# Kernel optimization log

Measured on AMD Instinct MI355X. Metric: run time of the kernel, lower is better.

The kernel has to match this reference:

```python
import jax, jax.numpy as jnp
import numpy as np

B, S, D = 2, 2048, 1024
H, HD = 16, 64  # num_heads, head_dim
EPS = 1e-6      # flax LayerNorm default
ROPE_BASE = 10000.0


def _layernorm(x, scale, bias=None, eps=EPS):
    mu = jnp.mean(x, axis=-1, keepdims=True)
    var = jnp.mean(jnp.square(x - mu), axis=-1, keepdims=True)
    y = (x - mu) * jax.lax.rsqrt(var + eps) * scale
    return y + bias if bias is not None else y


def _rotate_half(x):
    x1, x2 = x[..., : x.shape[-1] // 2], x[..., x.shape[-1] // 2 :]
    return jnp.concatenate((-x2, x1), axis=-1)


def _rope_tables(seq_len, head_dim, dtype):
    inv_freq = 1.0 / ROPE_BASE ** (jnp.arange(0, head_dim, 2, dtype=jnp.float32) / head_dim)
    t = jnp.arange(seq_len, dtype=jnp.float32)
    freqs = jnp.einsum('i,j->ij', t, inv_freq)          # [S, HD/2]
    emb = jnp.concatenate((freqs, freqs), axis=-1)      # [S, HD]
    return jnp.cos(emb).astype(dtype), jnp.sin(emb).astype(dtype)


def setup_inputs() -> dict:
    key = jax.random.key(0)
    ks = jax.random.split(key, 4)
    return {
        'x': jax.random.normal(ks[0], (B, S, D), dtype=jnp.float32),
        'w_qkv': jax.random.normal(ks[1], (D, 3 * D), dtype=jnp.float32) * (1.0 / np.sqrt(D)),
        'b_qkv': jnp.zeros((3 * D,), dtype=jnp.float32),
        'w_out': jax.random.normal(ks[2], (D, D), dtype=jnp.float32) * (0.1 / np.sqrt(D)),
        'b_out': jnp.zeros((D,), dtype=jnp.float32),
        'ln_scale': jnp.ones((D,), dtype=jnp.float32),
        'ln_bias': jnp.zeros((D,), dtype=jnp.float32),
        'q_scale': jnp.ones((HD,), dtype=jnp.float32),
        'k_scale': jnp.ones((HD,), dtype=jnp.float32),
    }


def reference(x, w_qkv, b_qkv, w_out, b_out, ln_scale, ln_bias, q_scale, k_scale):
    b, s, d = x.shape
    # input LayerNorm
    xn = _layernorm(x, ln_scale, ln_bias)
    # fused QKV projection
    qkv = xn @ w_qkv + b_qkv                              # [B, S, 3D]
    q, k, v = jnp.split(qkv, 3, axis=-1)
    def to_bhsd(t):
        return t.reshape(b, s, H, HD).transpose(0, 2, 1, 3)
    q, k, v = to_bhsd(q), to_bhsd(k), to_bhsd(v)          # [B, H, S, HD]
    # per-head QK LayerNorm (no bias)
    q = _layernorm(q, q_scale)
    k = _layernorm(k, k_scale)
    # RoPE
    cos, sin = _rope_tables(s, HD, q.dtype)               # [S, HD]
    cos, sin = cos[None, None], sin[None, None]
    q = q * cos + _rotate_half(q) * sin
    k = k * cos + _rotate_half(k) * sin
    # scaled dot-product attention (softmax over key positions)
    scale = 1.0 / np.sqrt(HD)
    scores = jnp.einsum('bhqd,bhkd->bhqk', q, k) * scale  # [B, H, S, S]
    probs = jax.nn.softmax(scores, axis=-1)
    attn = jnp.einsum('bhqk,bhkd->bhqd', probs, v)        # [B, H, S, HD]
    attn = attn.transpose(0, 2, 1, 3).reshape(b, s, d)
    return attn @ w_out + b_out
```

## Files before the change

### kernel.cpp

```cpp
#include <hip/hip_runtime.h>
#include <math.h>

#define BB 2
#define SS 2048
#define DD 1024
#define HH 16
#define HDD 64
static constexpr float EPS = 1e-6f;

typedef __bf16 bf16x8 __attribute__((ext_vector_type(8)));
typedef __bf16 bf16x4 __attribute__((ext_vector_type(4)));
typedef float f32x4 __attribute__((ext_vector_type(4)));
typedef __attribute__((address_space(1))) const unsigned int gas_u32;
typedef __attribute__((address_space(3))) unsigned int las_u32;

__device__ __forceinline__ unsigned short f2bf(float f) {
    unsigned int u = __float_as_uint(f);
    u = (u + 0x7FFFu + ((u >> 16) & 1u)) >> 16;
    return (unsigned short)u;
}

__device__ __forceinline__ uint2 pack4bf(float a, float b, float c, float d) {
    bf16x4 v;
    v[0] = (__bf16)a; v[1] = (__bf16)b; v[2] = (__bf16)c; v[3] = (__bf16)d;
    return *(uint2*)&v;
}

__device__ __forceinline__ void async_ld16(const unsigned short* g, unsigned short* l) {
    __builtin_amdgcn_global_load_lds((gas_u32*)g, (las_u32*)l, 16, 0, 0);
}

__global__ __launch_bounds__(256) void cast_transpose(const float* __restrict__ w,
                                                      unsigned short* __restrict__ wt,
                                                      int K, int N) {
    __shared__ float tile[32][36];
    const int n0 = blockIdx.x * 32;
    const int k0 = blockIdx.y * 32;
    const int t = threadIdx.x;
    const int r = t >> 3;
    const int c = (t & 7) * 4;
    *(float4*)&tile[r][c] = *(const float4*)(w + (size_t)(k0 + r) * N + n0 + c);
    __syncthreads();
    unsigned short o[4];
#pragma unroll
    for (int i = 0; i < 4; i++) o[i] = f2bf(tile[c + i][r]);
    *(uint2*)(wt + (size_t)(n0 + r) * K + k0 + c) = *(uint2*)o;
}

__global__ __launch_bounds__(256) void rope_tables(float* __restrict__ ctab,
                                                   float* __restrict__ stab) {
    const int idx = blockIdx.x * 256 + threadIdx.x;
    const int s = idx >> 5;
    const int i = idx & 31;
    const float ang = (float)s * exp2f(-(float)i * (13.287712379549449f / 32.f));
    ctab[idx] = cosf(ang);
    stab[idx] = sinf(ang);
}

__global__ __launch_bounds__(256) void ln_kernel(const float* __restrict__ x,
                                                 const float* __restrict__ scale,
                                                 const float* __restrict__ bias,
                                                 unsigned short* __restrict__ xn) {
    __shared__ float red[4];
    const int row = blockIdx.x;
    const int t = threadIdx.x;
    const float* xr = x + (size_t)row * DD + t * 4;

    float4 v = *(const float4*)xr;
    float s = v.x + v.y + v.z + v.w;
#pragma unroll
    for (int o = 32; o; o >>= 1) s += __shfl_xor(s, o);
    if ((t & 63) == 0) red[t >> 6] = s;
    __syncthreads();
    const float mu = (red[0] + red[1] + red[2] + red[3]) * (1.f / DD);

    float4 d = {v.x - mu, v.y - mu, v.z - mu, v.w - mu};
    float sq = d.x * d.x + d.y * d.y + d.z * d.z + d.w * d.w;
#pragma unroll
    for (int o = 32; o; o >>= 1) sq += __shfl_xor(sq, o);
    __syncthreads();
    if ((t & 63) == 0) red[t >> 6] = sq;
    __syncthreads();
    const float var = (red[0] + red[1] + red[2] + red[3]) * (1.f / DD);
    const float rstd = rsqrtf(var + EPS);

    const float4 sc = *(const float4*)(scale + t * 4);
    const float4 bi = *(const float4*)(bias + t * 4);
    unsigned short o[4];
    o[0] = f2bf(d.x * rstd * sc.x + bi.x);
    o[1] = f2bf(d.y * rstd * sc.y + bi.y);
    o[2] = f2bf(d.z * rstd * sc.z + bi.z);
    o[3] = f2bf(d.w * rstd * sc.w + bi.w);
    *(uint2*)(xn + (size_t)row * DD + t * 4) = *(uint2*)o;
}

__global__ __launch_bounds__(256) void gemm_mfma_bt(const unsigned short* __restrict__ A,
                                                    const unsigned short* __restrict__ Bt,
                                                    const float* __restrict__ bias,
                                                    float* __restrict__ C,
                                                    int M, int N, int K) {
    __shared__ __align__(16) unsigned short As[128][32];
    __shared__ __align__(16) unsigned short Bs[128][32];

    const int bm = blockIdx.y * 128;
    const int bn = blockIdx.x * 128;
    const int t = threadIdx.x;
    const int wv = t >> 6;
    const int ln = t & 63;
    const int m16 = ln & 15;
    const int quad = ln >> 4;
    const int wm = (wv >> 1) * 64;
    const int wn = (wv & 1) * 64;

    f32x4 acc[4][4];
#pragma unroll
    for (int i = 0; i < 4; i++)
#pragma unroll
        for (int j = 0; j < 4; j++) acc[i][j] = (f32x4){0.f, 0.f, 0.f, 0.f};

    const int srow = wv * 32 + (ln >> 2);
    const int sk = (ln & 3) * 8;
    const unsigned short* aptr = A + (size_t)(bm + srow) * K + sk;
    const unsigned short* bptr = Bt + (size_t)(bn + srow) * K + sk;
    unsigned short* al0 = &As[wv * 32][0];
    unsigned short* al1 = &As[wv * 32 + 16][0];
    unsigned short* bl0 = &Bs[wv * 32][0];
    unsigned short* bl1 = &Bs[wv * 32 + 16][0];

    for (int k0 = 0; k0 < K; k0 += 32) {
        __syncthreads();
        async_ld16(aptr, al0);
        async_ld16(aptr + 16 * (size_t)K, al1);
        async_ld16(bptr, bl0);
        async_ld16(bptr + 16 * (size_t)K, bl1);
        __syncthreads();

        bf16x8 af[4], bf[4];
#pragma unroll
        for (int i = 0; i < 4; i++)
            af[i] = *(const bf16x8*)&As[wm + i * 16 + m16][quad * 8];
#pragma unroll
        for (int j = 0; j < 4; j++)
            bf[j] = *(const bf16x8*)&Bs[wn + j * 16 + m16][quad * 8];
#pragma unroll
        for (int i = 0; i < 4; i++)
#pragma unroll
            for (int j = 0; j < 4; j++)
                acc[i][j] = __builtin_amdgcn_mfma_f32_16x16x32_bf16(af[i], bf[j], acc[i][j], 0, 0, 0);

        aptr += 32;
        bptr += 32;
    }

#pragma unroll
    for (int j = 0; j < 4; j++) {
        const int n = bn + wn + j * 16 + m16;
        const float bv = bias[n];
#pragma unroll
        for (int i = 0; i < 4; i++) {
            float* cp = C + (size_t)(bm + wm + i * 16 + quad * 4) * N + n;
#pragma unroll
            for (int r = 0; r < 4; r++)
                cp[(size_t)r * N] = acc[i][j][r] + bv;
        }
    }
}

__device__ __forceinline__ float wave_sum64(float x) {
#pragma unroll
    for (int o = 32; o; o >>= 1) x += __shfl_xor(x, o);
    return x;
}

__global__ __launch_bounds__(256) void head_ln_rope(const float* __restrict__ qkv,
                                                    const float* __restrict__ q_scale,
                                                    const float* __restrict__ k_scale,
                                                    const float* __restrict__ ctab,
                                                    const float* __restrict__ stab,
                                                    unsigned short* __restrict__ qt,
                                                    unsigned short* __restrict__ kt,
                                                    unsigned short* __restrict__ vt) {
    const int wave = (blockIdx.x * 256 + threadIdx.x) >> 6;
    const int lane = threadIdx.x & 63;
    const int h = wave & (HH - 1);
    const int row = wave >> 4;
    const int b = row >> 11;
    const int s = row & (SS - 1);

    const float* base = qkv + (size_t)row * (3 * DD) + h * HDD;
    const float qv = base[lane];
    const float kv = base[DD + lane];
    const float vv = base[2 * DD + lane];

    const float mq = wave_sum64(qv) * (1.f / 64.f);
    const float dq = qv - mq;
    const float varq = wave_sum64(dq * dq) * (1.f / 64.f);
    const float yq = dq * rsqrtf(varq + EPS) * q_scale[lane];

    const float mk = wave_sum64(kv) * (1.f / 64.f);
    const float dk = kv - mk;
    const float vark = wave_sum64(dk * dk) * (1.f / 64.f);
    const float yk = dk * rsqrtf(vark + EPS) * k_scale[lane];

    const int i = lane & 31;
    const float cv = ctab[s * 32 + i];
    const float sv = stab[s * 32 + i];
    const float pq = __shfl_xor(yq, 32);
    const float pk = __shfl_xor(yk, 32);
    const float rq = (lane < 32) ? -pq : pq;
    const float rk = (lane < 32) ? -pk : pk;
    const float oq = yq * cv + rq * sv;
    const float ok = yk * cv + rk * sv;

    const size_t oidx = (((size_t)(b * HH + h) * SS) + s) * HDD + lane;
    qt[oidx] = f2bf(oq * 0.18033688011112042f);
    kt[oidx] = f2bf(ok);
    vt[oidx] = f2bf(vv);
}

__global__ __launch_bounds__(256) void transpose_v(const unsigned short* __restrict__ vt,
                                                   unsigned short* __restrict__ vtT) {
    __shared__ unsigned short tile[64][72];
    const int bh = blockIdx.x >> 5;
    const int s0 = (blockIdx.x & 31) * 64;
    const int t = threadIdx.x;
    const int row = t >> 2;
    const int c0 = (t & 3) * 16;
    const unsigned short* src = vt + ((size_t)bh * SS + s0 + row) * HDD + c0;
    *(uint4*)&tile[row][c0]     = *(const uint4*)(src);
    *(uint4*)&tile[row][c0 + 8] = *(const uint4*)(src + 8);
    __syncthreads();
    unsigned short outv[16];
#pragma unroll
    for (int i = 0; i < 16; i++) outv[i] = tile[c0 + i][row];
    unsigned short* dst = vtT + ((size_t)bh * HDD + row) * SS + s0 + c0;
    *(uint4*)dst       = *(uint4*)&outv[0];
    *(uint4*)(dst + 8) = *(uint4*)&outv[8];
}

__global__ __launch_bounds__(256, 4) void attn_mfma(const unsigned short* __restrict__ qt,
                                                    const unsigned short* __restrict__ kt,
                                                    const unsigned short* __restrict__ vtT,
                                                    float* __restrict__ Opart,
                                                    float* __restrict__ lpart) {
    __shared__ __align__(16) unsigned short KsS[64 * 64];
    __shared__ __align__(16) unsigned short VsS[64 * 64];
    __shared__ __align__(16) unsigned short PbS[4][32 * 64];

    const int bh = blockIdx.x >> 4;
    const int q0 = (blockIdx.x & 15) * 128;
    const int ks = blockIdx.y;
    const int t = threadIdx.x;
    const int wq = t >> 6;
    const int lane = t & 63;
    const int m16 = lane & 15;
    const int quad = lane >> 4;
    const int m7 = m16 & 7;

    const int cs = quad ^ m7;
    const int koff = m16 * 64 + cs * 8;
    const int srow = t >> 2;
    const int sch = (t & 3) * 2;
    const int sw0 = srow * 64 + ((sch)     ^ (srow & 7)) * 8;
    const int sw1 = srow * 64 + ((sch + 1) ^ (srow & 7)) * 8;
    const int pwb = m16 * 64 + 4 * (quad & 1);
    const int qh = quad >> 1;

    bf16x8 qb[2][2];
#pragma unroll
    for (int u = 0; u < 2; u++) {
        const unsigned short* qp =
            qt + ((size_t)bh * SS + q0 + wq * 32 + u * 16 + m16) * HDD + quad * 8;
        qb[u][0] = *(const bf16x8*)qp;
        qb[u][1] = *(const bf16x8*)(qp + 32);
    }

    bf16x8 ones;
#pragma unroll
    for (int j = 0; j < 8; j++) ones[j] = (__bf16)1.0f;

    f32x4 O[2][4];
#pragma unroll
    for (int u = 0; u < 2; u++)
#pragma unroll
        for (int f = 0; f < 4; f++) O[u][f] = (f32x4){0.f, 0.f, 0.f, 0.f};
    f32x4 lacc[2] = {(f32x4){0.f, 0.f, 0.f, 0.f}, (f32x4){0.f, 0.f, 0.f, 0.f}};

    const unsigned short* kbase = kt + (size_t)bh * SS * HDD;
    const unsigned short* vbase = vtT + (size_t)bh * HDD * SS;
    const f32x4 cinit = (f32x4){-12.f, -12.f, -12.f, -12.f};

    const int kstart = ks * (SS / 2);
    for (int k0 = kstart; k0 < kstart + SS / 2; k0 += 64) {
        __syncthreads();
        {
            const unsigned short* ksrc = kbase + (size_t)(k0 + srow) * HDD + sch * 8;
            *(uint4*)&KsS[sw0] = *(const uint4*)ksrc;
            *(uint4*)&KsS[sw1] = *(const uint4*)(ksrc + 8);
            const unsigned short* vsrc = vbase + (size_t)srow * SS + k0 + sch * 8;
            *(uint4*)&VsS[sw0] = *(const uint4*)vsrc;
            *(uint4*)&VsS[sw1] = *(const uint4*)(vsrc + 8);
        }
        __syncthreads();

        f32x4 S[2][4];
#pragma unroll
        for (int g = 0; g < 4; g++) {
            const bf16x8 ka0 = *(const bf16x8*)&KsS[g * 1024 + koff];
            const bf16x8 ka1 = *(const bf16x8*)&KsS[g * 1024 + (koff ^ 32)];
#pragma unroll
            for (int u = 0; u < 2; u++) {
                f32x4 a = __builtin_amdgcn_mfma_f32_16x16x32_bf16(ka0, qb[u][0], cinit, 0, 0, 0);
                a = __builtin_amdgcn_mfma_f32_16x16x32_bf16(ka1, qb[u][1], a, 0, 0, 0);
                S[u][g] = a;
            }
        }

#pragma unroll
        for (int u = 0; u < 2; u++) {
#pragma unroll
            for (int g = 0; g < 4; g++) {
                const float p0 = exp2f(S[u][g][0]);
                const float p1 = exp2f(S[u][g][1]);
                const float p2 = exp2f(S[u][g][2]);
                const float p3 = exp2f(S[u][g][3]);
                *(uint2*)&PbS[wq][u * 1024 + pwb + ((2 * g + qh) ^ m7) * 8] =
                    pack4bf(p0, p1, p2, p3);
            }
        }
        asm volatile("s_waitcnt lgkmcnt(0)" ::: "memory");

        bf16x8 pb[2][2];
#pragma unroll
        for (int u = 0; u < 2; u++) {
            pb[u][0] = *(const bf16x8*)&PbS[wq][u * 1024 + koff];
            pb[u][1] = *(const bf16x8*)&PbS[wq][u * 1024 + (koff ^ 32)];
        }

#pragma unroll
        for (int u = 0; u < 2; u++) {
            lacc[u] = __builtin_amdgcn_mfma_f32_16x16x32_bf16(ones, pb[u][0], lacc[u], 0, 0, 0);
            lacc[u] = __builtin_amdgcn_mfma_f32_16x16x32_bf16(ones, pb[u][1], lacc[u], 0, 0, 0);
        }
#pragma unroll
        for (int f = 0; f < 4; f++) {
            const bf16x8 va0 = *(const bf16x8*)&VsS[f * 1024 + koff];
            const bf16x8 va1 = *(const bf16x8*)&VsS[f * 1024 + (koff ^ 32)];
#pragma unroll
            for (int u = 0; u < 2; u++) {
                O[u][f] = __builtin_amdgcn_mfma_f32_16x16x32_bf16(va0, pb[u][0], O[u][f], 0, 0, 0);
                O[u][f] = __builtin_amdgcn_mfma_f32_16x16x32_bf16(va1, pb[u][1], O[u][f], 0, 0, 0);
            }
        }
    }

    const int b_ = bh >> 4;
    const int h_ = bh & 15;
    float* obase0 = Opart + (size_t)ks * ((size_t)BB * SS * DD);
#pragma unroll
    for (int u = 0; u < 2; u++) {
        const int s_ = q0 + wq * 32 + u * 16 + m16;
        float* orow = obase0 + ((size_t)b_ * SS + s_) * DD + h_ * HDD;
#pragma unroll
        for (int f = 0; f < 4; f++)
            *(f32x4*)(orow + f * 16 + quad * 4) = O[u][f];
        if (quad == 0)
            lpart[ks * (32 * SS) + bh * SS + s_] = lacc[u][0];
    }
}

__global__ __launch_bounds__(256) void combine_attn(const float* __restrict__ Opart,
                                                    const float* __restrict__ lpart,
                                                    unsigned short* __restrict__ attn) {
    const int row = blockIdx.x;
    const int t = threadIdx.x;
    const int c = t * 4;
    const int h = t >> 4;
    const int b = row >> 11;
    const int s = row & (SS - 1);

    const size_t off = (size_t)row * DD + c;
    const float4 o0 = *(const float4*)(Opart + off);
    const float4 o1 = *(const float4*)(Opart + (size_t)BB * SS * DD + off);
    const int li = (b * HH + h) * SS + s;
    const float inv = 1.f / (lpart[li] + lpart[32 * SS + li]);

    *(uint2*)(attn + off) = pack4bf((o0.x + o1.x) * inv, (o0.y + o1.y) * inv,
                                    (o0.z + o1.z) * inv, (o0.w + o1.w) * inv);
}

extern "C" void kernel_launch(void* const* d_in, const int* in_sizes, int n_in,
                              void* d_out, int out_size, void* d_ws, size_t ws_size,
                              hipStream_t stream) {
    const float* x        = (const float*)d_in[0];
    const float* w_qkv    = (const float*)d_in[1];
    const float* b_qkv    = (const float*)d_in[2];
    const float* w_out    = (const float*)d_in[3];
    const float* b_out    = (const float*)d_in[4];
    const float* ln_scale = (const float*)d_in[5];
    const float* ln_bias  = (const float*)d_in[6];
    const float* q_scale  = (const float*)d_in[7];
    const float* k_scale  = (const float*)d_in[8];
    float* out = (float*)d_out;

    char* ws = (char*)d_ws;
    const size_t MB = 1024 * 1024;
    unsigned short* xn    = (unsigned short*)(ws + 0);
    float*          lpart = (float*)(ws + 8 * MB);
    float*          ctab  = (float*)(ws + 9 * MB);
    float*          stab  = (float*)(ws + 10 * MB);
    float*          qkv   = (float*)(ws + 16 * MB);
    float*          Opart = (float*)(ws + 16 * MB);
    unsigned short* wqkvT = (unsigned short*)(ws + 64 * MB);
    unsigned short* woutT = (unsigned short*)(ws + 70 * MB);
    unsigned short* qt    = (unsigned short*)(ws + 72 * MB);
    unsigned short* kt    = (unsigned short*)(ws + 80 * MB);
    unsigned short* vt    = (unsigned short*)(ws + 88 * MB);
    unsigned short* vtT   = (unsigned short*)(ws + 96 * MB);
    unsigned short* attn  = (unsigned short*)(ws + 104 * MB);

    const int M = BB * SS;

    cast_transpose<<<dim3(3 * DD / 32, DD / 32), 256, 0, stream>>>(w_qkv, wqkvT, DD, 3 * DD);
    cast_transpose<<<dim3(DD / 32, DD / 32), 256, 0, stream>>>(w_out, woutT, DD, DD);
    rope_tables<<<SS * 32 / 256, 256, 0, stream>>>(ctab, stab);

    ln_kernel<<<M, 256, 0, stream>>>(x, ln_scale, ln_bias, xn);

    gemm_mfma_bt<<<dim3(3 * DD / 128, M / 128), 256, 0, stream>>>(xn, wqkvT, b_qkv, qkv,
                                                                  M, 3 * DD, DD);

    head_ln_rope<<<M * HH / 4, 256, 0, stream>>>(qkv, q_scale, k_scale, ctab, stab,
                                                 qt, kt, vt);

    transpose_v<<<BB * HH * (SS / 64), 256, 0, stream>>>(vt, vtT);

    attn_mfma<<<dim3(BB * HH * (SS / 128), 2), 256, 0, stream>>>(qt, kt, vtT, Opart, lpart);

    combine_attn<<<M, 256, 0, stream>>>(Opart, lpart, attn);

    gemm_mfma_bt<<<dim3(DD / 128, M / 128), 256, 0, stream>>>(attn, woutT, b_out, out,
                                                              M, DD, DD);
}
```

Measured before the change: 251.9 us.

## Store QKV as bf16, load K/V directly in attention, narrow out-proj tiles

The QKV GEMM now writes bf16 instead of fp32, halving the intermediate traffic, and head_ln_rope reads bf16 and passes V through unchanged. The attention kernel drops its LDS staging of K and V tiles and their barriers, loading MFMA operands straight from global memory or cache. The output projection uses a new 128x64 tile GEMM so more blocks launch for N=1024. Costs are an extra bf16 rounding of Q/K before the head LayerNorm and uncoalesced, repeated global loads of K/V in attention.

```diff
diff --git a/kernel.cpp b/kernel.cpp
--- a/kernel.cpp
+++ b/kernel.cpp
@@ -18,6 +18,10 @@
     unsigned int u = __float_as_uint(f);
     u = (u + 0x7FFFu + ((u >> 16) & 1u)) >> 16;
     return (unsigned short)u;
+}
+
+__device__ __forceinline__ float b2f(unsigned short u) {
+    return __uint_as_float((unsigned int)u << 16);
 }
 
 __device__ __forceinline__ uint2 pack4bf(float a, float b, float c, float d) {
@@ -94,11 +98,11 @@
     *(uint2*)(xn + (size_t)row * DD + t * 4) = *(uint2*)o;
 }
 
-__global__ __launch_bounds__(256) void gemm_mfma_bt(const unsigned short* __restrict__ A,
-                                                    const unsigned short* __restrict__ Bt,
-                                                    const float* __restrict__ bias,
-                                                    float* __restrict__ C,
-                                                    int M, int N, int K) {
+__global__ __launch_bounds__(256) void gemm_mfma_bt_bf16(const unsigned short* __restrict__ A,
+                                                         const unsigned short* __restrict__ Bt,
+                                                         const float* __restrict__ bias,
+                                                         unsigned short* __restrict__ C,
+                                                         int M, int N, int K) {
     __shared__ __align__(16) unsigned short As[128][32];
     __shared__ __align__(16) unsigned short Bs[128][32];
 
@@ -158,6 +162,76 @@
         const float bv = bias[n];
 #pragma unroll
         for (int i = 0; i < 4; i++) {
+            unsigned short* cp = C + (size_t)(bm + wm + i * 16 + quad * 4) * N + n;
+#pragma unroll
+            for (int r = 0; r < 4; r++)
+                cp[(size_t)r * N] = f2bf(acc[i][j][r] + bv);
+        }
+    }
+}
+
+__global__ __launch_bounds__(256) void gemm_mfma_bt_n64(const unsigned short* __restrict__ A,
+                                                        const unsigned short* __restrict__ Bt,
+                                                        const float* __restrict__ bias,
+                                                        float* __restrict__ C,
+                                                        int M, int N, int K) {
+    __shared__ __align__(16) unsigned short As[128][32];
+    __shared__ __align__(16) unsigned short Bs[64][32];
+
+    const int bm = blockIdx.y * 128;
+    const int bn = blockIdx.x * 64;
+    const int t = threadIdx.x;
+    const int wv = t >> 6;
+    const int ln = t & 63;
+    const int m16 = ln & 15;
+    const int quad = ln >> 4;
+    const int wm = (wv >> 1) * 64;
+    const int wn = (wv & 1) * 32;
+
+    f32x4 acc[4][2];
+#pragma unroll
+    for (int i = 0; i < 4; i++)
+#pragma unroll
+        for (int j = 0; j < 2; j++) acc[i][j] = (f32x4){0.f, 0.f, 0.f, 0.f};
+
+    const int sr = ln >> 2;
+    const int sk = (ln & 3) * 8;
+    const unsigned short* aptr = A + (size_t)(bm + wv * 32 + sr) * K + sk;
+    const unsigned short* bptr = Bt + (size_t)(bn + wv * 16 + sr) * K + sk;
+    unsigned short* al0 = &As[wv * 32][0];
+    unsigned short* al1 = &As[wv * 32 + 16][0];
+    unsigned short* bl0 = &Bs[wv * 16][0];
+
+    for (int k0 = 0; k0 < K; k0 += 32) {
+        __syncthreads();
+        async_ld16(aptr, al0);
+        async_ld16(aptr + 16 * (size_t)K, al1);
+        async_ld16(bptr, bl0);
+        __syncthreads();
+
+        bf16x8 af[4], bf[2];
+#pragma unroll
+        for (int i = 0; i < 4; i++)
+            af[i] = *(const bf16x8*)&As[wm + i * 16 + m16][quad * 8];
+#pragma unroll
+        for (int j = 0; j < 2; j++)
+            bf[j] = *(const bf16x8*)&Bs[wn + j * 16 + m16][quad * 8];
+#pragma unroll
+        for (int i = 0; i < 4; i++)
+#pragma unroll
+            for (int j = 0; j < 2; j++)
+                acc[i][j] = __builtin_amdgcn_mfma_f32_16x16x32_bf16(af[i], bf[j], acc[i][j], 0, 0, 0);
+
+        aptr += 32;
+        bptr += 32;
+    }
+
+#pragma unroll
+    for (int j = 0; j < 2; j++) {
+        const int n = bn + wn + j * 16 + m16;
+        const float bv = bias[n];
+#pragma unroll
+        for (int i = 0; i < 4; i++) {
             float* cp = C + (size_t)(bm + wm + i * 16 + quad * 4) * N + n;
 #pragma unroll
             for (int r = 0; r < 4; r++)
@@ -172,7 +246,7 @@
     return x;
 }
 
-__global__ __launch_bounds__(256) void head_ln_rope(const float* __restrict__ qkv,
+__global__ __launch_bounds__(256) void head_ln_rope(const unsigned short* __restrict__ qkv,
                                                     const float* __restrict__ q_scale,
                                                     const float* __restrict__ k_scale,
                                                     const float* __restrict__ ctab,
@@ -187,10 +261,10 @@
     const int b = row >> 11;
     const int s = row & (SS - 1);
 
-    const float* base = qkv + (size_t)row * (3 * DD) + h * HDD;
-    const float qv = base[lane];
-    const float kv = base[DD + lane];
-    const float vv = base[2 * DD + lane];
+    const unsigned short* base = qkv + (size_t)row * (3 * DD) + h * HDD;
+    const float qv = b2f(base[lane]);
+    const float kv = b2f(base[DD + lane]);
+    const unsigned short vv = base[2 * DD + lane];
 
     const float mq = wave_sum64(qv) * (1.f / 64.f);
     const float dq = qv - mq;
@@ -215,7 +289,7 @@
     const size_t oidx = (((size_t)(b * HH + h) * SS) + s) * HDD + lane;
     qt[oidx] = f2bf(oq * 0.18033688011112042f);
     kt[oidx] = f2bf(ok);
-    vt[oidx] = f2bf(vv);
+    vt[oidx] = vv;
 }
 
 __global__ __launch_bounds__(256) void transpose_v(const unsigned short* __restrict__ vt,
@@ -243,8 +317,6 @@
                                                     const unsigned short* __restrict__ vtT,
                                                     float* __restrict__ Opart,
                                                     float* __restrict__ lpart) {
-    __shared__ __align__(16) unsigned short KsS[64 * 64];
-    __shared__ __align__(16) unsigned short VsS[64 * 64];
     __shared__ __align__(16) unsigned short PbS[4][32 * 64];
 
     const int bh = blockIdx.x >> 4;
@@ -257,12 +329,7 @@
     const int quad = lane >> 4;
     const int m7 = m16 & 7;
 
-    const int cs = quad ^ m7;
-    const int koff = m16 * 64 + cs * 8;
-    const int srow = t >> 2;
-    const int sch = (t & 3) * 2;
-    const int sw0 = srow * 64 + ((sch)     ^ (srow & 7)) * 8;
-    const int sw1 = srow * 64 + ((sch + 1) ^ (srow & 7)) * 8;
+    const int koff = m16 * 64 + (quad ^ m7) * 8;
     const int pwb = m16 * 64 + 4 * (quad & 1);
     const int qh = quad >> 1;
 
@@ -292,28 +359,26 @@
 
     const int kstart = ks * (SS / 2);
     for (int k0 = kstart; k0 < kstart + SS / 2; k0 += 64) {
-        __syncthreads();
-        {
-            const unsigned short* ksrc = kbase + (size_t)(k0 + srow) * HDD + sch * 8;
-            *(uint4*)&KsS[sw0] = *(const uint4*)ksrc;
-            *(uint4*)&KsS[sw1] = *(const uint4*)(ksrc + 8);
-            const unsigned short* vsrc = vbase + (size_t)srow * SS + k0 + sch * 8;
-            *(uint4*)&VsS[sw0] = *(const uint4*)vsrc;
-            *(uint4*)&VsS[sw1] = *(const uint4*)(vsrc + 8);
-        }
-        __syncthreads();
-
+        const unsigned short* kb = kbase + (size_t)(k0 + m16) * HDD + quad * 8;
         f32x4 S[2][4];
 #pragma unroll
         for (int g = 0; g < 4; g++) {
-            const bf16x8 ka0 = *(const bf16x8*)&KsS[g * 1024 + koff];
-            const bf16x8 ka1 = *(const bf16x8*)&KsS[g * 1024 + (koff ^ 32)];
+            const bf16x8 ka0 = *(const bf16x8*)(kb + g * 16 * HDD);
+            const bf16x8 ka1 = *(const bf16x8*)(kb + g * 16 * HDD + 32);
 #pragma unroll
             for (int u = 0; u < 2; u++) {
                 f32x4 a = __builtin_amdgcn_mfma_f32_16x16x32_bf16(ka0, qb[u][0], cinit, 0, 0, 0);
                 a = __builtin_amdgcn_mfma_f32_16x16x32_bf16(ka1, qb[u][1], a, 0, 0, 0);
                 S[u][g] = a;
             }
+        }
+
+        const unsigned short* vb = vbase + (size_t)m16 * SS + k0 + quad * 8;
+        bf16x8 va[4][2];
+#pragma unroll
+        for (int f = 0; f < 4; f++) {
+            va[f][0] = *(const bf16x8*)(vb + (size_t)f * 16 * SS);
+            va[f][1] = *(const bf16x8*)(vb + (size_t)f * 16 * SS + 32);
         }
 
 #pragma unroll
@@ -344,12 +409,10 @@
         }
 #pragma unroll
         for (int f = 0; f < 4; f++) {
-            const bf16x8 va0 = *(const bf16x8*)&VsS[f * 1024 + koff];
-            const bf16x8 va1 = *(const bf16x8*)&VsS[f * 1024 + (koff ^ 32)];
 #pragma unroll
             for (int u = 0; u < 2; u++) {
-                O[u][f] = __builtin_amdgcn_mfma_f32_16x16x32_bf16(va0, pb[u][0], O[u][f], 0, 0, 0);
-                O[u][f] = __builtin_amdgcn_mfma_f32_16x16x32_bf16(va1, pb[u][1], O[u][f], 0, 0, 0);
+                O[u][f] = __builtin_amdgcn_mfma_f32_16x16x32_bf16(va[f][0], pb[u][0], O[u][f], 0, 0, 0);
+                O[u][f] = __builtin_amdgcn_mfma_f32_16x16x32_bf16(va[f][1], pb[u][1], O[u][f], 0, 0, 0);
             }
         }
     }
@@ -409,7 +472,7 @@
     float*          lpart = (float*)(ws + 8 * MB);
     float*          ctab  = (float*)(ws + 9 * MB);
     float*          stab  = (float*)(ws + 10 * MB);
-    float*          qkv   = (float*)(ws + 16 * MB);
+    unsigned short* qkv   = (unsigned short*)(ws + 16 * MB);
     float*          Opart = (float*)(ws + 16 * MB);
     unsigned short* wqkvT = (unsigned short*)(ws + 64 * MB);
     unsigned short* woutT = (unsigned short*)(ws + 70 * MB);
@@ -427,8 +490,8 @@
 
     ln_kernel<<<M, 256, 0, stream>>>(x, ln_scale, ln_bias, xn);
 
-    gemm_mfma_bt<<<dim3(3 * DD / 128, M / 128), 256, 0, stream>>>(xn, wqkvT, b_qkv, qkv,
-                                                                  M, 3 * DD, DD);
+    gemm_mfma_bt_bf16<<<dim3(3 * DD / 128, M / 128), 256, 0, stream>>>(xn, wqkvT, b_qkv,
+                                                                       qkv, M, 3 * DD, DD);
 
     head_ln_rope<<<M * HH / 4, 256, 0, stream>>>(qkv, q_scale, k_scale, ctab, stab,
                                                  qt, kt, vt);
@@ -439,6 +502,6 @@
 
     combine_attn<<<M, 256, 0, stream>>>(Opart, lpart, attn);
 
-    gemm_mfma_bt<<<dim3(DD / 128, M / 128), 256, 0, stream>>>(attn, woutT, b_out, out,
-                                                              M, DD, DD);
-}
+    gemm_mfma_bt_n64<<<dim3(DD / 64, M / 128), 256, 0, stream>>>(attn, woutT, b_out, out,
+                                                                 M, DD, DD);
+}
```

Result: slower. 324.4 us (+28.8%).
